# Performance work log

Measured on AMD Instinct MI355X. Metric: run time of the kernel, lower is better.

The kernel has to match this reference:

```python
import jax, jax.numpy as jnp
import numpy as np

HEADS, DIM_HEAD, C, B, HS, WS = 8, 64, 512, 2, 48, 48


def setup_inputs() -> dict:
    key = jax.random.key(0)
    ks = jax.random.split(key, 9)
    s = 0.02
    return {
        "hidden_states": jax.random.normal(ks[0], (B, C, HS, WS), jnp.float32),
        "Wq": jax.random.normal(ks[1], (HEADS, DIM_HEAD, C), jnp.float32) * s,
        "bq": jax.random.normal(ks[2], (HEADS, DIM_HEAD), jnp.float32) * s,
        "Wk": jax.random.normal(ks[3], (HEADS, DIM_HEAD, C), jnp.float32) * s,
        "bk": jax.random.normal(ks[4], (HEADS, DIM_HEAD), jnp.float32) * s,
        "Wv": jax.random.normal(ks[5], (HEADS, DIM_HEAD, C), jnp.float32) * s,
        "bv": jax.random.normal(ks[6], (HEADS, DIM_HEAD), jnp.float32) * s,
        "Wo": jax.random.normal(ks[7], (C, HEADS * DIM_HEAD), jnp.float32) * s,
        "bo": jax.random.normal(ks[8], (C,), jnp.float32) * s,
    }


def reference(hidden_states, Wq, bq, Wk, bk, Wv, bv, Wo, bo):
    # hidden_states: [B, C, H, W]; per-head 1x1 convs == per-head linear over C.
    b, c, h, w = hidden_states.shape
    hw = h * w
    x = hidden_states.reshape(b, c, hw)  # [B, C, HW]
    # Batched per-head projections (fuses the per-head Conv2d loop).
    q = jnp.einsum('bcs,ndc->bnsd', x, Wq) + bq[None, :, None, :]  # [B, n, HW, d]
    k = jnp.einsum('bcs,ndc->bnsd', x, Wk) + bk[None, :, None, :]
    v = jnp.einsum('bcs,ndc->bnsd', x, Wv) + bv[None, :, None, :]
    scale = 1.0 / jnp.sqrt(jnp.asarray(DIM_HEAD, hidden_states.dtype))
    scores = jnp.einsum('bnqd,bnkd->bnqk', q, k) * scale  # [B, n, HW, HW]
    probs = jax.nn.softmax(scores, axis=-1)
    attn = jnp.einsum('bnqk,bnkd->bnqd', probs, v)  # [B, n, HW, d]
    # concat heads along last dim (matches torch.cat(..., dim=-1))
    attn = attn.transpose(0, 2, 1, 3).reshape(b, hw, HEADS * DIM_HEAD)
    out = attn @ Wo.T + bo  # [B, HW, C] (to_out[0]; to_out[1] dropout = identity)
    out = out.reshape(b, h, w, c).transpose(0, 3, 1, 2)  # [B, C, H, W]
    return out
```

## Files before the change

kernel.cpp:

```cpp
#include <hip/hip_runtime.h>
#include <hip/hip_bf16.h>

#define HEADS 8
#define DHEAD 64
#define CDIM  512
#define SEQ   2304
#define ND    512

typedef unsigned short u16;
typedef unsigned int   u32;
typedef __attribute__((ext_vector_type(8))) short short8;
typedef __attribute__((ext_vector_type(4))) float f32x4;

#define QSCALE 0.18033688011112043f

__device__ __forceinline__ u16 f2bf(float f) {
    union { float f; u32 u; } x; x.f = f;
    u32 r = x.u + 0x7FFFu + ((x.u >> 16) & 1u);
    return (u16)(r >> 16);
}
__device__ __forceinline__ float bf2f(u16 v) {
    union { u32 u; float f; } x; x.u = ((u32)v) << 16; return x.f;
}
__device__ __forceinline__ u32 pkbf(float a, float b) {
    union { float f; u32 u; } x, y; x.f = a; y.f = b;
    return __builtin_amdgcn_perm(y.u + 0x8000u, x.u + 0x8000u, 0x07060302u);
}
__device__ __forceinline__ f32x4 mfma16(short8 a, short8 b, f32x4 c) {
    return __builtin_amdgcn_mfma_f32_16x16x32_bf16(a, b, c, 0, 0, 0);
}
__device__ __forceinline__ void cp16(const void* g, void* l) {
    __builtin_amdgcn_global_load_lds(
        (const __attribute__((address_space(1))) u32*)(uintptr_t)g,
        (__attribute__((address_space(3))) u32*)(u32)(uintptr_t)l,
        16, 0, 0);
}
__device__ __forceinline__ int kperm_inv(int r) {
    return (r & ~0x1C) | ((r & 0x0C) << 1) | ((r & 0x10) >> 2);
}

__global__ void prep_kernel(const float* __restrict__ H,
                            const float* __restrict__ Wq, const float* __restrict__ Wk,
                            const float* __restrict__ Wv, const float* __restrict__ Wo,
                            u16* __restrict__ Wqkv, u16* __restrict__ Wob,
                            u16* __restrict__ X) {
    __shared__ float tile[32][33];
    const int t = threadIdx.x;
    const int bx = blockIdx.x;
    if (bx < 4096) {
        int idx = bx * 256 + t;
        const int N1 = CDIM * ND;
        if (idx < N1)             Wqkv[idx] = f2bf(Wq[idx]);
        else if (idx < 2 * N1)    Wqkv[idx] = f2bf(Wk[idx - N1]);
        else if (idx < 3 * N1)    Wqkv[idx] = f2bf(Wv[idx - 2 * N1]);
        else                      Wob[idx - 3 * N1] = f2bf(Wo[idx - 3 * N1]);
    } else {
        int bb = bx - 4096;
        int st = bb % 72, ct = (bb / 72) % 16, b = bb / (72 * 16);
        int tx = t & 31, ty = t >> 5;
#pragma unroll
        for (int k = 0; k < 4; ++k) {
            int c = ct * 32 + ty + k * 8;
            tile[ty + k * 8][tx] = H[((size_t)b * CDIM + c) * SEQ + st * 32 + tx];
        }
        __syncthreads();
#pragma unroll
        for (int k = 0; k < 4; ++k) {
            int s = st * 32 + ty + k * 8;
            X[((size_t)b * SEQ + s) * CDIM + ct * 32 + tx] = f2bf(tile[tx][ty + k * 8]);
        }
    }
}

__global__ __launch_bounds__(256) void gemm_qkv_kernel(
        const u16* __restrict__ W, const u16* __restrict__ X,
        const float* __restrict__ bq, const float* __restrict__ bk, const float* __restrict__ bv,
        u16* __restrict__ Q, u16* __restrict__ K, u16* __restrict__ V) {
    __shared__ __align__(16) u16 sm[2 * (64 * 64 + 128 * 64)];
    const int n0 = blockIdx.x * 128;
    const int m0 = blockIdx.y * 64;
    const int b  = blockIdx.z;
    const int t = threadIdx.x;
    const int lane = t & 63, w = t >> 6;
    const int l16 = lane & 15, quad = lane >> 4;
    const int x7 = l16 & 7;
    const int srow = t >> 3, scol = (t & 7) * 8;
    const int scol_sw = ((t & 7) ^ (srow & 7)) * 8;
    const u16* Xb = X + (size_t)b * SEQ * CDIM;

    f32x4 acc[4][2] = {};

    {
        u16* As = sm; u16* Bs = sm + 64 * 64;
#pragma unroll
        for (int it = 0; it < 2; ++it) {
            int r2 = it * 32 + srow;
            cp16(&W[(size_t)(m0 + r2) * 512 + scol_sw], &As[r2 * 64 + scol]);
        }
#pragma unroll
        for (int it = 0; it < 4; ++it) {
            int r2 = it * 32 + srow;
            cp16(&Xb[(size_t)(n0 + r2) * 512 + scol_sw], &Bs[r2 * 64 + scol]);
        }
    }
    for (int kb = 0; kb < 512; kb += 64) {
        const int pb = (kb >> 6) & 1;
        u16* As = sm + pb * 12288;
        u16* Bs = As + 64 * 64;
        __syncthreads();
        if (kb + 64 < 512) {
            u16* An = sm + (pb ^ 1) * 12288;
            u16* Bn = An + 64 * 64;
#pragma unroll
            for (int it = 0; it < 2; ++it) {
                int r2 = it * 32 + srow;
                cp16(&W[(size_t)(m0 + r2) * 512 + kb + 64 + scol_sw], &An[r2 * 64 + scol]);
            }
#pragma unroll
            for (int it = 0; it < 4; ++it) {
                int r2 = it * 32 + srow;
                cp16(&Xb[(size_t)(n0 + r2) * 512 + kb + 64 + scol_sw], &Bn[r2 * 64 + scol]);
            }
        }
#pragma unroll
        for (int kk = 0; kk < 2; ++kk) {
            const int co = ((kk * 4 + quad) ^ x7) * 8;
            short8 af[4], bfr[2];
#pragma unroll
            for (int i = 0; i < 4; ++i)
                af[i] = *(const short8*)&As[(i * 16 + l16) * 64 + co];
#pragma unroll
            for (int j = 0; j < 2; ++j)
                bfr[j] = *(const short8*)&Bs[(w * 32 + j * 16 + l16) * 64 + co];
#pragma unroll
            for (int i = 0; i < 4; ++i)
#pragma unroll
                for (int j = 0; j < 2; ++j)
                    acc[i][j] = mfma16(af[i], bfr[j], acc[i][j]);
        }
    }

    if (m0 < 1024) {
        const bool isQ = (m0 < 512);
        const float* bias = isQ ? bq : bk;
        const float sc = isQ ? QSCALE : 1.0f;
        const int mq = isQ ? m0 : m0 - 512;
        u16* dst = isQ ? Q : K;
#pragma unroll
        for (int j = 0; j < 2; ++j) {
            int s = n0 + w * 32 + j * 16 + l16;
#pragma unroll
            for (int i = 0; i < 4; ++i) {
                int mm = mq + i * 16 + quad * 4;
                uint2 val;
                val.x = pkbf((acc[i][j][0] + bias[mm + 0]) * sc, (acc[i][j][1] + bias[mm + 1]) * sc);
                val.y = pkbf((acc[i][j][2] + bias[mm + 2]) * sc, (acc[i][j][3] + bias[mm + 3]) * sc);
                *(uint2*)&dst[(((size_t)(b * 8 + (mm >> 6))) * SEQ + s) * 64 + (mm & 63)] = val;
            }
        }
    } else {
#pragma unroll
        for (int j = 0; j < 2; ++j) {
            int s = n0 + w * 32 + j * 16 + l16;
#pragma unroll
            for (int i = 0; i < 4; ++i) {
                int mbase = m0 - 1024 + i * 16 + quad * 4;
#pragma unroll
                for (int r = 0; r < 4; ++r) {
                    int mm = mbase + r;
                    V[((size_t)(b * 512 + mm)) * SEQ + s] = f2bf(acc[i][j][r] + bv[mm]);
                }
            }
        }
    }
}

__global__ __launch_bounds__(256) void attn_partial(
        const u16* __restrict__ Q,
        const u16* __restrict__ K,
        const u16* __restrict__ Vt,
        u16* __restrict__ Opart,
        float* __restrict__ Lpart) {
    __shared__ __align__(16) u16 sm[2 * 8192];
    const int pair = blockIdx.x & 15, qt = blockIdx.x >> 4;
    const int c = blockIdx.y;
    const int b = pair >> 3, h = pair & 7;
    const int t = threadIdx.x, lane = t & 63, w = t >> 6;
    const int l16 = lane & 15, quad = lane >> 4;
    const int x7 = l16 & 7;
    const int srow = t >> 3;
    const int scol = (t & 7) * 8;
    const int scol_sw = ((t & 7) ^ (srow & 7)) * 8;
    const int kinv0 = kperm_inv(srow), kinv1 = kperm_inv(32 + srow);
    const int cA = (quad ^ x7) * 8;
    const int cB = (quad ^ x7 ^ 4) * 8;

    const u16* Qg = Q + ((size_t)pair * SEQ + qt * 128) * 64;
    const int rA = w * 16 + l16, rB = 64 + rA;
    short8 qfa0 = *(const short8*)&Qg[(size_t)rA * 64 + quad * 8];
    short8 qfa1 = *(const short8*)&Qg[(size_t)rA * 64 + 32 + quad * 8];
    short8 qfb0 = *(const short8*)&Qg[(size_t)rB * 64 + quad * 8];
    short8 qfb1 = *(const short8*)&Qg[(size_t)rB * 64 + 32 + quad * 8];

    const u16* Kg = K  + ((size_t)pair * SEQ + c * 576) * 64;
    const u16* Vg = Vt + ((size_t)(b * 512 + h * 64)) * SEQ + c * 576;

    f32x4 laccA = {0.f, 0.f, 0.f, 0.f}, laccB = {0.f, 0.f, 0.f, 0.f};
    f32x4 oA[4] = {}, oB[4] = {};

    {
        u16* Ks = sm; u16* Vs = sm + 4096;
        cp16(&Kg[(size_t)kinv0 * 64 + scol_sw], &Ks[srow * 64 + scol]);
        cp16(&Kg[(size_t)kinv1 * 64 + scol_sw], &Ks[(32 + srow) * 64 + scol]);
        cp16(&Vg[(size_t)srow * SEQ + scol_sw],        &Vs[srow * 64 + scol]);
        cp16(&Vg[(size_t)(32 + srow) * SEQ + scol_sw], &Vs[(32 + srow) * 64 + scol]);
    }
    for (int kt = 0; kt < 9; ++kt) {
        const int pb = kt & 1;
        const u16* Ks = sm + pb * 8192;
        const u16* Vs = Ks + 4096;
        __syncthreads();
        if (kt < 8) {
            u16* Kn = sm + (pb ^ 1) * 8192;
            u16* Vn = Kn + 4096;
            cp16(&Kg[(size_t)((kt + 1) * 64 + kinv0) * 64 + scol_sw], &Kn[srow * 64 + scol]);
            cp16(&Kg[(size_t)((kt + 1) * 64 + kinv1) * 64 + scol_sw], &Kn[(32 + srow) * 64 + scol]);
            cp16(&Vg[(size_t)srow * SEQ + (kt + 1) * 64 + scol_sw],        &Vn[srow * 64 + scol]);
            cp16(&Vg[(size_t)(32 + srow) * SEQ + (kt + 1) * 64 + scol_sw], &Vn[(32 + srow) * 64 + scol]);
        }
        f32x4 saccA[4] = {}, saccB[4] = {};
#pragma unroll
        for (int j = 0; j < 4; ++j) {
            short8 kf0 = *(const short8*)&Ks[(j * 16 + l16) * 64 + cA];
            short8 kf1 = *(const short8*)&Ks[(j * 16 + l16) * 64 + cB];
            saccA[j] = mfma16(kf0, qfa0, saccA[j]);
            saccA[j] = mfma16(kf1, qfa1, saccA[j]);
            saccB[j] = mfma16(kf0, qfb0, saccB[j]);
            saccB[j] = mfma16(kf1, qfb1, saccB[j]);
        }
        float pA[4][4], pB[4][4];
#pragma unroll
        for (int j = 0; j < 4; ++j)
#pragma unroll
            for (int r = 0; r < 4; ++r) {
                pA[j][r] = __builtin_amdgcn_exp2f(saccA[j][r]);
                laccA[j] += pA[j][r];
                pB[j][r] = __builtin_amdgcn_exp2f(saccB[j][r]);
                laccB[j] += pB[j][r];
            }
#pragma unroll
        for (int g = 0; g < 2; ++g) {
            short8 pfA, pfB;
            u32* pwA = (u32*)&pfA;
            u32* pwB = (u32*)&pfB;
            pwA[0] = pkbf(pA[2 * g][0], pA[2 * g][1]);
            pwA[1] = pkbf(pA[2 * g][2], pA[2 * g][3]);
            pwA[2] = pkbf(pA[2 * g + 1][0], pA[2 * g + 1][1]);
            pwA[3] = pkbf(pA[2 * g + 1][2], pA[2 * g + 1][3]);
            pwB[0] = pkbf(pB[2 * g][0], pB[2 * g][1]);
            pwB[1] = pkbf(pB[2 * g][2], pB[2 * g][3]);
            pwB[2] = pkbf(pB[2 * g + 1][0], pB[2 * g + 1][1]);
            pwB[3] = pkbf(pB[2 * g + 1][2], pB[2 * g + 1][3]);
            const int cg = g ? cB : cA;
#pragma unroll
            for (int i = 0; i < 4; ++i) {
                short8 vf = *(const short8*)&Vs[(i * 16 + l16) * 64 + cg];
                oA[i] = mfma16(vf, pfA, oA[i]);
                oB[i] = mfma16(vf, pfB, oB[i]);
            }
        }
    }
    float lA = laccA[0] + laccA[1] + laccA[2] + laccA[3];
    lA += __shfl_xor(lA, 16); lA += __shfl_xor(lA, 32);
    float lB = laccB[0] + laccB[1] + laccB[2] + laccB[3];
    lB += __shfl_xor(lB, 16); lB += __shfl_xor(lB, 32);
    float invA = 1.0f / lA, invB = 1.0f / lB;
    const size_t orow = ((size_t)(c * 16 + pair)) * SEQ + qt * 128;

    __syncthreads();
#pragma unroll
    for (int i = 0; i < 4; ++i) {
        uint2 pka, pkb;
        pka.x = pkbf(oA[i][0] * invA, oA[i][1] * invA);
        pka.y = pkbf(oA[i][2] * invA, oA[i][3] * invA);
        pkb.x = pkbf(oB[i][0] * invB, oB[i][1] * invB);
        pkb.y = pkbf(oB[i][2] * invB, oB[i][3] * invB);
        *(uint2*)&sm[(w * 16 + l16) * 72 + i * 16 + quad * 4] = pka;
        *(uint2*)&sm[(64 + w * 16 + l16) * 72 + i * 16 + quad * 4] = pkb;
    }
    if (quad == 0) {
        Lpart[orow + w * 16 + l16] = lA;
        Lpart[orow + 64 + w * 16 + l16] = lB;
    }
    __syncthreads();
#pragma unroll
    for (int it = 0; it < 4; ++it) {
        int v = it * 256 + t;
        int row = v >> 3, col = (v & 7) * 8;
        *(uint4*)&Opart[(orow + row) * 64 + col] = *(const uint4*)&sm[row * 72 + col];
    }
}

__global__ __launch_bounds__(256) void attn_combine(
        const u16* __restrict__ Opart, const float* __restrict__ Lpart,
        u16* __restrict__ At) {
    const int bid = blockIdx.x;
    const int pair = bid / 144, sb = bid % 144;
    const int tid = threadIdx.x;
    const int rl = tid >> 4, dg = tid & 15;
    const int s = sb * 16 + rl;
    const int b = pair >> 3, h = pair & 7;
    float wc[4], L = 0.f;
#pragma unroll
    for (int c = 0; c < 4; ++c) {
        wc[c] = Lpart[(size_t)(c * 16 + pair) * SEQ + s];
        L += wc[c];
    }
    float invL = 1.0f / L;
    float acc[4] = {0.f, 0.f, 0.f, 0.f};
#pragma unroll
    for (int c = 0; c < 4; ++c) {
        ushort4 v = *(const ushort4*)&Opart[((size_t)(c * 16 + pair) * SEQ + s) * 64 + dg * 4];
        acc[0] += wc[c] * bf2f(v.x);
        acc[1] += wc[c] * bf2f(v.y);
        acc[2] += wc[c] * bf2f(v.z);
        acc[3] += wc[c] * bf2f(v.w);
    }
    uint2 outv;
    outv.x = pkbf(acc[0] * invL, acc[1] * invL);
    outv.y = pkbf(acc[2] * invL, acc[3] * invL);
    *(uint2*)&At[((size_t)b * SEQ + s) * ND + h * 64 + dg * 4] = outv;
}

__global__ __launch_bounds__(256) void gemm_out_kernel(
        const u16* __restrict__ Wob, const u16* __restrict__ At,
        const float* __restrict__ bo, float* __restrict__ out) {
    __shared__ __align__(16) u16 sm[2 * 8192];
    const int n0 = blockIdx.x * 64;
    const int m0 = blockIdx.y * 64;
    const int b  = blockIdx.z;
    const int t = threadIdx.x;
    const int lane = t & 63, w = t >> 6;
    const int l16 = lane & 15, quad = lane >> 4;
    const int x7 = l16 & 7;
    const int srow = t >> 3, scol = (t & 7) * 8;
    const int scol_sw = ((t & 7) ^ (srow & 7)) * 8;
    const u16* Ab = At + (size_t)b * SEQ * ND;

    f32x4 acc[4] = {};

    {
        u16* As = sm; u16* Bs = sm + 4096;
#pragma unroll
        for (int it = 0; it < 2; ++it) {
            int r2 = it * 32 + srow;
            cp16(&Wob[(size_t)(m0 + r2) * 512 + scol_sw], &As[r2 * 64 + scol]);
            cp16(&Ab [(size_t)(n0 + r2) * 512 + scol_sw], &Bs[r2 * 64 + scol]);
        }
    }
    for (int kb = 0; kb < 512; kb += 64) {
        const int pb = (kb >> 6) & 1;
        const u16* As = sm + pb * 8192;
        const u16* Bs = As + 4096;
        __syncthreads();
        if (kb + 64 < 512) {
            u16* An = sm + (pb ^ 1) * 8192;
            u16* Bn = An + 4096;
#pragma unroll
            for (int it = 0; it < 2; ++it) {
                int r2 = it * 32 + srow;
                cp16(&Wob[(size_t)(m0 + r2) * 512 + kb + 64 + scol_sw], &An[r2 * 64 + scol]);
                cp16(&Ab [(size_t)(n0 + r2) * 512 + kb + 64 + scol_sw], &Bn[r2 * 64 + scol]);
            }
        }
#pragma unroll
        for (int kk = 0; kk < 2; ++kk) {
            const int co = ((kk * 4 + quad) ^ x7) * 8;
            short8 af[4];
#pragma unroll
            for (int i = 0; i < 4; ++i)
                af[i] = *(const short8*)&As[(i * 16 + l16) * 64 + co];
            short8 bfr = *(const short8*)&Bs[(w * 16 + l16) * 64 + co];
#pragma unroll
            for (int i = 0; i < 4; ++i)
                acc[i] = mfma16(af[i], bfr, acc[i]);
        }
    }
#pragma unroll
    for (int i = 0; i < 4; ++i) {
        int cbase = m0 + i * 16 + quad * 4;
        int s = n0 + w * 16 + l16;
#pragma unroll
        for (int r = 0; r < 4; ++r) {
            int cc = cbase + r;
            out[((size_t)(b * 512 + cc)) * SEQ + s] = acc[i][r] + bo[cc];
        }
    }
}

extern "C" void kernel_launch(void* const* d_in, const int* in_sizes, int n_in,
                              void* d_out, int out_size, void* d_ws, size_t ws_size,
                              hipStream_t stream) {
    const float* H  = (const float*)d_in[0];
    const float* Wq = (const float*)d_in[1];
    const float* bq = (const float*)d_in[2];
    const float* Wk = (const float*)d_in[3];
    const float* bk = (const float*)d_in[4];
    const float* Wv = (const float*)d_in[5];
    const float* bv = (const float*)d_in[6];
    const float* Wo = (const float*)d_in[7];
    const float* bo = (const float*)d_in[8];
    float* out = (float*)d_out;

    u16* ws    = (u16*)d_ws;
    u16* Wqkv  = ws;
    u16* Wob   = Wqkv  + 1536 * 512;
    u16* Xbf   = Wob   + 512 * 512;
    u16* Qb    = Xbf   + 2 * SEQ * CDIM;
    u16* Kb    = Qb    + 2 * SEQ * ND;
    u16* Vb    = Kb    + 2 * SEQ * ND;
    u16* At    = Vb    + 2 * SEQ * ND;
    u16* Opart = At    + 2 * SEQ * ND;
    float* Lpart = (float*)(Opart + 4 * 16 * SEQ * 64);

    prep_kernel<<<6400, 256, 0, stream>>>(H, Wq, Wk, Wv, Wo, Wqkv, Wob, Xbf);
    gemm_qkv_kernel<<<dim3(18, 24, 2), 256, 0, stream>>>(Wqkv, Xbf, bq, bk, bv, Qb, Kb, Vb);
    attn_partial<<<dim3(288, 4), 256, 0, stream>>>(Qb, Kb, Vb, Opart, Lpart);
    attn_combine<<<2304, 256, 0, stream>>>(Opart, Lpart, At);
    gemm_out_kernel<<<dim3(36, 8, 2), 256, 0, stream>>>(Wob, At, bo, out);
}
```

Measured before the change: 135.8 us.

## Enlarge attention query tile to 192 rows per block for K/V reuse

Each attn_partial block now processes 192 query rows (three 64-row groups per wave set) instead of 128, so every K/V tile staged in shared memory feeds more MFMAs and the grid shrinks from 288x4 to 192x4 blocks. Launch bounds request 3 blocks per SM, and the softmax/pack code is reorganised to compute exp and bf16 packing per group. The trade-off is higher register pressure from 12 output accumulators per lane, and fewer blocks to fill the GPU's compute units. The epilogue staging buffer reuses shared memory sized for 192 rows at a 72-element stride.

```diff
diff --git a/kernel.cpp b/kernel.cpp
--- a/kernel.cpp
+++ b/kernel.cpp
@@ -175,7 +175,7 @@
     }
 }
 
-__global__ __launch_bounds__(256) void attn_partial(
+__global__ __launch_bounds__(256, 3) void attn_partial(
         const u16* __restrict__ Q,
         const u16* __restrict__ K,
         const u16* __restrict__ Vt,
@@ -195,18 +195,20 @@
     const int cA = (quad ^ x7) * 8;
     const int cB = (quad ^ x7 ^ 4) * 8;
 
-    const u16* Qg = Q + ((size_t)pair * SEQ + qt * 128) * 64;
-    const int rA = w * 16 + l16, rB = 64 + rA;
-    short8 qfa0 = *(const short8*)&Qg[(size_t)rA * 64 + quad * 8];
-    short8 qfa1 = *(const short8*)&Qg[(size_t)rA * 64 + 32 + quad * 8];
-    short8 qfb0 = *(const short8*)&Qg[(size_t)rB * 64 + quad * 8];
-    short8 qfb1 = *(const short8*)&Qg[(size_t)rB * 64 + 32 + quad * 8];
+    const u16* Qg = Q + ((size_t)pair * SEQ + qt * 192) * 64;
+    const int rA = w * 16 + l16;
+    short8 qf[3][2];
+#pragma unroll
+    for (int G = 0; G < 3; ++G) {
+        qf[G][0] = *(const short8*)&Qg[(size_t)(G * 64 + rA) * 64 + quad * 8];
+        qf[G][1] = *(const short8*)&Qg[(size_t)(G * 64 + rA) * 64 + 32 + quad * 8];
+    }
 
     const u16* Kg = K  + ((size_t)pair * SEQ + c * 576) * 64;
     const u16* Vg = Vt + ((size_t)(b * 512 + h * 64)) * SEQ + c * 576;
 
-    f32x4 laccA = {0.f, 0.f, 0.f, 0.f}, laccB = {0.f, 0.f, 0.f, 0.f};
-    f32x4 oA[4] = {}, oB[4] = {};
+    float lacc[3] = {0.f, 0.f, 0.f};
+    f32x4 o[3][4] = {};
 
     {
         u16* Ks = sm; u16* Vs = sm + 4096;
@@ -228,73 +230,74 @@
             cp16(&Vg[(size_t)srow * SEQ + (kt + 1) * 64 + scol_sw],        &Vn[srow * 64 + scol]);
             cp16(&Vg[(size_t)(32 + srow) * SEQ + (kt + 1) * 64 + scol_sw], &Vn[(32 + srow) * 64 + scol]);
         }
-        f32x4 saccA[4] = {}, saccB[4] = {};
+        f32x4 sacc[3][4];
 #pragma unroll
         for (int j = 0; j < 4; ++j) {
             short8 kf0 = *(const short8*)&Ks[(j * 16 + l16) * 64 + cA];
             short8 kf1 = *(const short8*)&Ks[(j * 16 + l16) * 64 + cB];
-            saccA[j] = mfma16(kf0, qfa0, saccA[j]);
-            saccA[j] = mfma16(kf1, qfa1, saccA[j]);
-            saccB[j] = mfma16(kf0, qfb0, saccB[j]);
-            saccB[j] = mfma16(kf1, qfb1, saccB[j]);
-        }
-        float pA[4][4], pB[4][4];
-#pragma unroll
-        for (int j = 0; j < 4; ++j)
-#pragma unroll
-            for (int r = 0; r < 4; ++r) {
-                pA[j][r] = __builtin_amdgcn_exp2f(saccA[j][r]);
-                laccA[j] += pA[j][r];
-                pB[j][r] = __builtin_amdgcn_exp2f(saccB[j][r]);
-                laccB[j] += pB[j][r];
+#pragma unroll
+            for (int G = 0; G < 3; ++G) {
+                f32x4 z = {0.f, 0.f, 0.f, 0.f};
+                z = mfma16(kf0, qf[G][0], z);
+                sacc[G][j] = mfma16(kf1, qf[G][1], z);
+            }
+        }
+        u32 pk[3][8];
+#pragma unroll
+        for (int G = 0; G < 3; ++G)
+#pragma unroll
+            for (int j = 0; j < 4; ++j) {
+                float e0 = __builtin_amdgcn_exp2f(sacc[G][j][0]);
+                float e1 = __builtin_amdgcn_exp2f(sacc[G][j][1]);
+                float e2 = __builtin_amdgcn_exp2f(sacc[G][j][2]);
+                float e3 = __builtin_amdgcn_exp2f(sacc[G][j][3]);
+                lacc[G] += (e0 + e1) + (e2 + e3);
+                pk[G][2 * j]     = pkbf(e0, e1);
+                pk[G][2 * j + 1] = pkbf(e2, e3);
             }
 #pragma unroll
         for (int g = 0; g < 2; ++g) {
-            short8 pfA, pfB;
-            u32* pwA = (u32*)&pfA;
-            u32* pwB = (u32*)&pfB;
-            pwA[0] = pkbf(pA[2 * g][0], pA[2 * g][1]);
-            pwA[1] = pkbf(pA[2 * g][2], pA[2 * g][3]);
-            pwA[2] = pkbf(pA[2 * g + 1][0], pA[2 * g + 1][1]);
-            pwA[3] = pkbf(pA[2 * g + 1][2], pA[2 * g + 1][3]);
-            pwB[0] = pkbf(pB[2 * g][0], pB[2 * g][1]);
-            pwB[1] = pkbf(pB[2 * g][2], pB[2 * g][3]);
-            pwB[2] = pkbf(pB[2 * g + 1][0], pB[2 * g + 1][1]);
-            pwB[3] = pkbf(pB[2 * g + 1][2], pB[2 * g + 1][3]);
             const int cg = g ? cB : cA;
 #pragma unroll
             for (int i = 0; i < 4; ++i) {
                 short8 vf = *(const short8*)&Vs[(i * 16 + l16) * 64 + cg];
-                oA[i] = mfma16(vf, pfA, oA[i]);
-                oB[i] = mfma16(vf, pfB, oB[i]);
-            }
-        }
-    }
-    float lA = laccA[0] + laccA[1] + laccA[2] + laccA[3];
-    lA += __shfl_xor(lA, 16); lA += __shfl_xor(lA, 32);
-    float lB = laccB[0] + laccB[1] + laccB[2] + laccB[3];
-    lB += __shfl_xor(lB, 16); lB += __shfl_xor(lB, 32);
-    float invA = 1.0f / lA, invB = 1.0f / lB;
-    const size_t orow = ((size_t)(c * 16 + pair)) * SEQ + qt * 128;
+#pragma unroll
+                for (int G = 0; G < 3; ++G) {
+                    short8 pf;
+                    u32* pw = (u32*)&pf;
+                    pw[0] = pk[G][4 * g + 0];
+                    pw[1] = pk[G][4 * g + 1];
+                    pw[2] = pk[G][4 * g + 2];
+                    pw[3] = pk[G][4 * g + 3];
+                    o[G][i] = mfma16(vf, pf, o[G][i]);
+                }
+            }
+        }
+    }
+    float linv[3];
+#pragma unroll
+    for (int G = 0; G < 3; ++G) {
+        float lr = lacc[G];
+        lr += __shfl_xor(lr, 16);
+        lr += __shfl_xor(lr, 32);
+        if (quad == 0) Lpart[((size_t)(c * 16 + pair)) * SEQ + qt * 192 + G * 64 + rA] = lr;
+        linv[G] = 1.0f / lr;
+    }
+    const size_t orow = ((size_t)(c * 16 + pair)) * SEQ + qt * 192;
 
     __syncthreads();
 #pragma unroll
-    for (int i = 0; i < 4; ++i) {
-        uint2 pka, pkb;
-        pka.x = pkbf(oA[i][0] * invA, oA[i][1] * invA);
-        pka.y = pkbf(oA[i][2] * invA, oA[i][3] * invA);
-        pkb.x = pkbf(oB[i][0] * invB, oB[i][1] * invB);
-        pkb.y = pkbf(oB[i][2] * invB, oB[i][3] * invB);
-        *(uint2*)&sm[(w * 16 + l16) * 72 + i * 16 + quad * 4] = pka;
-        *(uint2*)&sm[(64 + w * 16 + l16) * 72 + i * 16 + quad * 4] = pkb;
-    }
-    if (quad == 0) {
-        Lpart[orow + w * 16 + l16] = lA;
-        Lpart[orow + 64 + w * 16 + l16] = lB;
-    }
+    for (int G = 0; G < 3; ++G)
+#pragma unroll
+        for (int i = 0; i < 4; ++i) {
+            uint2 pkv;
+            pkv.x = pkbf(o[G][i][0] * linv[G], o[G][i][1] * linv[G]);
+            pkv.y = pkbf(o[G][i][2] * linv[G], o[G][i][3] * linv[G]);
+            *(uint2*)&sm[(G * 64 + rA) * 72 + i * 16 + quad * 4] = pkv;
+        }
     __syncthreads();
 #pragma unroll
-    for (int it = 0; it < 4; ++it) {
+    for (int it = 0; it < 6; ++it) {
         int v = it * 256 + t;
         int row = v >> 3, col = (v & 7) * 8;
         *(uint4*)&Opart[(orow + row) * 64 + col] = *(const uint4*)&sm[row * 72 + col];
@@ -425,7 +428,7 @@
 
     prep_kernel<<<6400, 256, 0, stream>>>(H, Wq, Wk, Wv, Wo, Wqkv, Wob, Xbf);
     gemm_qkv_kernel<<<dim3(18, 24, 2), 256, 0, stream>>>(Wqkv, Xbf, bq, bk, bv, Qb, Kb, Vb);
-    attn_partial<<<dim3(288, 4), 256, 0, stream>>>(Qb, Kb, Vb, Opart, Lpart);
+    attn_partial<<<dim3(192, 4), 256, 0, stream>>>(Qb, Kb, Vb, Opart, Lpart);
     attn_combine<<<2304, 256, 0, stream>>>(Opart, Lpart, At);
     gemm_out_kernel<<<dim3(36, 8, 2), 256, 0, stream>>>(Wob, At, bo, out);
 }
```

Result: no change. 135.0 us (-0.6%).
